# Kernel tuning notes

Measured on AMD Instinct MI355X. Metric: run time of the kernel, lower is better.

## Reference

```python
import jax, jax.numpy as jnp
import numpy as np

DIM = 768; HEADS = 12; N_PH = 4; EXPERTS = 8; TOPK = 2; EXPERT_DIM = 3072; MEM_HEADS = 8; EPS = 1e-5


def phm_linear(x, A, S, b):
    # PHM linear: W = sum_i kron(A[i] (n,n), S[i] (out/n, in/n)) -> (out, in); y = x @ W.T + b
    out_f = A.shape[1] * S.shape[1]
    in_f = A.shape[2] * S.shape[2]
    W = jnp.einsum('iab,icd->acbd', A, S).reshape(out_f, in_f)
    return x @ W.T + b


def layernorm(x, g, b):
    m = x.mean(-1, keepdims=True)
    v = x.var(-1, keepdims=True)
    return (x - m) / jnp.sqrt(v + EPS) * g + b


def quantum_attn(x, A_qkv, S_qkv, b_qkv, A_p, S_p, b_p, w_sup, w_ent):
    B, N, C = x.shape
    hd = C // HEADS
    qkv = phm_linear(x, A_qkv, S_qkv, b_qkv).reshape(B, N, 3, HEADS, hd)
    qkv = qkv.transpose(2, 0, 3, 1, 4)  # (3,B,H,N,hd)
    q, k, v = qkv[0], qkv[1], qkv[2]
    attn = jnp.einsum('bhnd,bhmd->bhnm', q, k) * (hd ** -0.5)
    # superposition head-mixing: sup[:,i] = sum_j w_sup[i,j] * attn[:,j]
    sup = jnp.einsum('ij,bjnm->binm', w_sup, attn)
    # entanglement: ent[:,i] = tanh(sup[:,i] + sum_j w_ent[i,j] * sup[:,j])
    ent = jnp.tanh(sup + jnp.einsum('ij,bjnm->binm', w_ent, sup))
    a = jax.nn.softmax(ent, axis=-1)
    o = jnp.einsum('bhnm,bhmd->bnhd', a, v).reshape(B, N, C)
    return phm_linear(o, A_p, S_p, b_p)


def moe(x, rA, rS, rb, domain_routing, domain_id, eA, eS, eb, ndw, ndb):
    logits = phm_linear(x, rA, rS, rb) + domain_routing[domain_id]  # (B,N,E)
    topv, topi = jax.lax.top_k(logits, TOPK)
    w = jax.nn.softmax(topv, axis=-1)  # (B,N,K)
    onehot = (topi[..., None] == jnp.arange(EXPERTS)).astype(x.dtype)  # (B,N,K,E)
    gates = jnp.einsum('bnk,bnke->bne', w, onehot)  # combined top-k gate per expert

    def expert(Ae, Se, be, We, bne):
        h = jax.nn.gelu(phm_linear(x, Ae, Se, be), approximate=False)
        return h @ We.T + bne

    outs = jax.vmap(expert)(eA, eS, eb, ndw, ndb)  # (E,B,N,C)
    return jnp.einsum('bne,ebnc->bnc', gates, outs)


def mem_mha(x, mem, iw, ib, ow, ob):
    # standard MHA: queries from x (B,N,C), keys/values from memory bank (M,C) shared across batch
    B, N, C = x.shape
    dh = C // MEM_HEADS
    q = (x @ iw[:C].T + ib[:C]).reshape(B, N, MEM_HEADS, dh)
    k = (mem @ iw[C:2 * C].T + ib[C:2 * C]).reshape(-1, MEM_HEADS, dh)
    v = (mem @ iw[2 * C:].T + ib[2 * C:]).reshape(-1, MEM_HEADS, dh)
    a = jax.nn.softmax(jnp.einsum('bnhd,mhd->bhnm', q, k) * (dh ** -0.5), axis=-1)
    o = jnp.einsum('bhnm,mhd->bnhd', a, v).reshape(B, N, C)
    return o @ ow.T + ob


def fractal(x, mems, iw, ib, ow, ob, pw, pb):
    # recursive FractalMemoryBank unrolled for depth=3:
    # level l: a_l = proc_l(MHA_l(prev, mem_l)); return prev + deeper(a_l)
    a0 = mem_mha(x, mems[0], iw[0], ib[0], ow[0], ob[0]) @ pw[0].T + pb[0]
    a1 = mem_mha(a0, mems[1], iw[1], ib[1], ow[1], ob[1]) @ pw[1].T + pb[1]
    a2 = mem_mha(a1, mems[2], iw[2], ib[2], ow[2], ob[2]) @ pw[2].T + pb[2]
    return x + (a0 + (a1 + a2))


def _fwd(x, ln1_g, ln1_b, attn_qkv_A, attn_qkv_S, attn_qkv_b, attn_proj_A, attn_proj_S, attn_proj_b,
         w_sup, w_ent, ln2_g, ln2_b, router_A, router_S, router_b, domain_routing,
         exp_A, exp_S, exp_b, exp_nd_w, exp_nd_b, mem0, mem1, mem2,
         mha_in_w, mha_in_b, mha_out_w, mha_out_b, proc_w, proc_b, ln3_g, ln3_b, domain_id):
    attended = x + quantum_attn(layernorm(x, ln1_g, ln1_b), attn_qkv_A, attn_qkv_S, attn_qkv_b,
                                attn_proj_A, attn_proj_S, attn_proj_b, w_sup, w_ent)
    moe_out = moe(layernorm(attended, ln2_g, ln2_b), router_A, router_S, router_b,
                  domain_routing, domain_id, exp_A, exp_S, exp_b, exp_nd_w, exp_nd_b)
    eo = attended + moe_out
    mo = fractal(eo, (mem0, mem1, mem2), mha_in_w, mha_in_b, mha_out_w, mha_out_b, proc_w, proc_b)
    return layernorm(mo, ln3_g, ln3_b)


def setup_inputs():
    key = jax.random.key(0)
    ks = iter(jax.random.split(key, 40))

    def rn(shape, s=0.02):
        return s * jax.random.normal(next(ks), shape, dtype=jnp.float32)

    B, N = 4, 512
    ones = jnp.ones(DIM, jnp.float32)
    zeros = jnp.zeros(DIM, jnp.float32)
    return {
        'x': rn((B, N, DIM), 1.0),
        'ln1_g': ones, 'ln1_b': zeros, 'ln2_g': ones, 'ln2_b': zeros, 'ln3_g': ones, 'ln3_b': zeros,
        'attn_qkv_A': rn((N_PH, N_PH, N_PH), 0.3),
        'attn_qkv_S': rn((N_PH, 3 * DIM // N_PH, DIM // N_PH)),
        'attn_qkv_b': jnp.zeros(3 * DIM, jnp.float32),
        'attn_proj_A': rn((N_PH, N_PH, N_PH), 0.3),
        'attn_proj_S': rn((N_PH, DIM // N_PH, DIM // N_PH)),
        'attn_proj_b': zeros,
        'w_sup': rn((HEADS, HEADS), 0.2), 'w_ent': rn((HEADS, HEADS), 0.2),
        'router_A': rn((N_PH, N_PH, N_PH), 0.3),
        'router_S': rn((N_PH, EXPERTS // N_PH, DIM // N_PH)),
        'router_b': jnp.zeros(EXPERTS, jnp.float32),
        'domain_routing': rn((6, EXPERTS), 1.0),
        'exp_A': rn((EXPERTS, N_PH, N_PH, N_PH), 0.3),
        'exp_S': rn((EXPERTS, N_PH, EXPERT_DIM // N_PH, DIM // N_PH)),
        'exp_b': jnp.zeros((EXPERTS, EXPERT_DIM), jnp.float32),
        'exp_nd_w': rn((EXPERTS, DIM, EXPERT_DIM)),
        'exp_nd_b': jnp.zeros((EXPERTS, DIM), jnp.float32),
        'mem0': rn((64, DIM), 1.0), 'mem1': rn((128, DIM), 1.0), 'mem2': rn((256, DIM), 1.0),
        'mha_in_w': rn((3, 3 * DIM, DIM)), 'mha_in_b': jnp.zeros((3, 3 * DIM), jnp.float32),
        'mha_out_w': rn((3, DIM, DIM)), 'mha_out_b': jnp.zeros((3, DIM), jnp.float32),
        'proc_w': rn((3, DIM, DIM)), 'proc_b': jnp.zeros((3, DIM), jnp.float32),
        'domain_id': 2,
    }


def reference(x, ln1_g, ln1_b, ln2_g, ln2_b, ln3_g, ln3_b, attn_qkv_A, attn_qkv_S, attn_qkv_b,
              attn_proj_A, attn_proj_S, attn_proj_b, w_sup, w_ent, router_A, router_S, router_b,
              domain_routing, exp_A, exp_S, exp_b, exp_nd_w, exp_nd_b, mem0, mem1, mem2,
              mha_in_w, mha_in_b, mha_out_w, mha_out_b, proc_w, proc_b, domain_id):
    return _fwd(x, ln1_g, ln1_b, attn_qkv_A, attn_qkv_S, attn_qkv_b, attn_proj_A, attn_proj_S,
                attn_proj_b, w_sup, w_ent, ln2_g, ln2_b, router_A, router_S, router_b,
                domain_routing, exp_A, exp_S, exp_b, exp_nd_w, exp_nd_b, mem0, mem1, mem2,
                mha_in_w, mha_in_b, mha_out_w, mha_out_b, proc_w, proc_b, ln3_g, ln3_b, domain_id)
```

## Files before the change

kernel.cpp:

```cpp
#include <hip/hip_runtime.h>
#include <math.h>

#define DIM    768
#define NTOK   2048
#define NSEQ   512
#define NBATCH 4
#define NHEADS 12
#define HD     64
#define QKVC   2304
#define MHEADS 8
#define MHD    96
#define NEXP   8
#define EDIM   3072
#define DD     (DIM*DIM)

typedef unsigned short u16;
typedef __attribute__((ext_vector_type(8))) short short8;
typedef __attribute__((ext_vector_type(4))) float f32x4;

struct L3 { long a, b, c; };
struct I3 { int a, b, c; };
struct CJ { const float4* s[6]; ushort4* d[6]; int n4[6]; };

__device__ __forceinline__ float gelu_exact(float v){
    return 0.5f * v * (1.f + erff(v * 0.70710678118654752f));
}
__device__ __forceinline__ u16 f2bf(float f){
    unsigned int u = __builtin_bit_cast(unsigned int, f);
    unsigned int r = (u + 0x7FFFu + ((u >> 16) & 1u)) >> 16;
    return (u16)r;
}
__device__ __forceinline__ float fast_tanh(float s){
    return 1.f - 2.f/(__expf(2.f*s) + 1.f);
}
__device__ __forceinline__ void gll16(const u16* g, u16* l){
    __builtin_amdgcn_global_load_lds((const __attribute__((address_space(1))) void*)g,
                                     (__attribute__((address_space(3))) void*)l, 16, 0, 0);
}

template<int WM,int WN,int FR>
__device__ __forceinline__ void mgemm_core(
    const u16* __restrict__ Xb, int ldx, int rowBase, int rowLim,
    const u16* __restrict__ Wb, int ldw, int colBase, int colLim, int K,
    const float* __restrict__ bias,
    const float* __restrict__ res, int ldres,
    float* __restrict__ Cf, u16* __restrict__ Cb, int ldc,
    float scale, int act)
{
    constexpr int TM = 16*FR;
    constexpr int RM = WM*TM, RN = WN*TM, NT = WM*WN*64;
    constexpr int IA = (RM*8)/NT, IB = (RN*8)/NT;
    __shared__ u16 As[2][RM*64];
    __shared__ u16 Bs[2][RN*64];
    int tid = threadIdx.x;
    int lane = tid & 63, w = tid >> 6;
    int wm = (w / WN) * TM, wn = (w % WN) * TM;
    const f32x4 zf = {0.f, 0.f, 0.f, 0.f};
    f32x4 acc[FR][FR];
    #pragma unroll
    for (int i=0;i<FR;i++)
        #pragma unroll
        for (int j=0;j<FR;j++) acc[i][j] = zf;

    const bool fullA = (rowBase + RM <= rowLim);
    const bool fullB = (colBase + RN <= colLim);
    const int nt = (K + 63) >> 6;

    auto stage = [&](int buf, int k0){
        const bool kfull = (k0 + 64 <= K);
        if (fullA && kfull) {
            #pragma unroll
            for (int it = 0; it < IA; ++it) {
                int idx = it*NT + tid;
                int r = idx >> 3, c = idx & 7;
                gll16(&Xb[(size_t)(rowBase + r)*ldx + k0 + ((c ^ (r & 7)) << 3)], &As[buf][(size_t)idx*8]);
            }
        } else {
            #pragma unroll
            for (int it = 0; it < IA; ++it) {
                int idx = it*NT + tid;
                int r = idx >> 3, c = idx & 7;
                int gr = rowBase + r;
                uint4 v = {0u,0u,0u,0u};
                if (gr < rowLim && (k0 + c*8) < K) v = *(const uint4*)&Xb[(size_t)gr*ldx + k0 + c*8];
                *(uint4*)&As[buf][r*64 + ((c ^ (r & 7)) * 8)] = v;
            }
        }
        if (fullB && kfull) {
            #pragma unroll
            for (int it = 0; it < IB; ++it) {
                int idx = it*NT + tid;
                int r = idx >> 3, c = idx & 7;
                gll16(&Wb[(size_t)(colBase + r)*ldw + k0 + ((c ^ (r & 7)) << 3)], &Bs[buf][(size_t)idx*8]);
            }
        } else {
            #pragma unroll
            for (int it = 0; it < IB; ++it) {
                int idx = it*NT + tid;
                int r = idx >> 3, c = idx & 7;
                int gc = colBase + r;
                uint4 v = {0u,0u,0u,0u};
                if (gc < colLim && (k0 + c*8) < K) v = *(const uint4*)&Wb[(size_t)gc*ldw + k0 + c*8];
                *(uint4*)&Bs[buf][r*64 + ((c ^ (r & 7)) * 8)] = v;
            }
        }
    };

    stage(0, 0);
    __syncthreads();
    for (int t = 0; t < nt; ++t) {
        if (t + 1 < nt) stage((t+1)&1, (t+1)*64);
        const u16* Ac = As[t&1];
        const u16* Bc = Bs[t&1];
        int lr = lane & 15, lk = lane >> 4;
        #pragma unroll
        for (int ks = 0; ks < 2; ++ks) {
            short8 af[FR], bfr[FR];
            #pragma unroll
            for (int mi=0; mi<FR; mi++){
                int row = wm + mi*16 + lr;
                int cidx = (ks*4 + lk) ^ (row & 7);
                af[mi] = *(const short8*)&Ac[row*64 + cidx*8];
            }
            #pragma unroll
            for (int ni=0; ni<FR; ni++){
                int col = wn + ni*16 + lr;
                int cidx = (ks*4 + lk) ^ (col & 7);
                bfr[ni] = *(const short8*)&Bc[col*64 + cidx*8];
            }
            #pragma unroll
            for (int mi=0; mi<FR; mi++)
                #pragma unroll
                for (int ni=0; ni<FR; ni++)
                    acc[mi][ni] = __builtin_amdgcn_mfma_f32_16x16x32_bf16(af[mi], bfr[ni], acc[mi][ni], 0, 0, 0);
        }
        __syncthreads();
    }
    int lr = lane & 15, lg = lane >> 4;
    #pragma unroll
    for (int mi=0; mi<FR; mi++){
        #pragma unroll
        for (int r=0; r<4; r++){
            int row = rowBase + wm + mi*16 + lg*4 + r;
            if (row >= rowLim) continue;
            #pragma unroll
            for (int ni=0; ni<FR; ni++){
                int col = colBase + wn + ni*16 + lr;
                if (col >= colLim) continue;
                float v = acc[mi][ni][r] * scale;
                if (bias) v += bias[col];
                if (act == 1) v = gelu_exact(v);
                if (Cb) Cb[(size_t)row*ldc + col] = f2bf(v);
                if (res) v += res[(size_t)row*ldres + col];
                if (Cf) Cf[(size_t)row*ldc + col] = v;
            }
        }
    }
}

template<int WM,int WN,int FR>
__global__ __launch_bounds__(WM*WN*64) void k_mgemm(
    const u16* __restrict__ X, int ldx, int M,
    const u16* __restrict__ W, int ldw, int N, int K,
    const float* __restrict__ bias, const float* __restrict__ res, int ldres,
    float* __restrict__ Cf, u16* __restrict__ Cb, int ldc, float scale, int act)
{
    constexpr int RM = WM*16*FR, RN = WN*16*FR;
    mgemm_core<WM,WN,FR>(X, ldx, blockIdx.x*RM, M, W, ldw, blockIdx.y*RN, N, K,
                         bias, res, ldres, Cf, Cb, ldc, scale, act);
}

template<int WM,int WN,int FR>
__global__ __launch_bounds__(WM*WN*64) void k_mgemm_b3(
    const u16* __restrict__ X, L3 xo, int ldx, I3 Mv,
    const u16* __restrict__ W, L3 wo, int ldw, int N, int K,
    const float* __restrict__ bias, L3 bo,
    u16* __restrict__ Cb, L3 co, int ldc, float scale, int act)
{
    constexpr int RM = WM*16*FR, RN = WN*16*FR;
    int z = blockIdx.z;
    int M    = (z==0) ? Mv.a : (z==1) ? Mv.b : Mv.c;
    long xof = (z==0) ? xo.a : (z==1) ? xo.b : xo.c;
    long wof = (z==0) ? wo.a : (z==1) ? wo.b : wo.c;
    long bof = (z==0) ? bo.a : (z==1) ? bo.b : bo.c;
    long cof = (z==0) ? co.a : (z==1) ? co.b : co.c;
    if ((int)blockIdx.x * RM >= M) return;
    mgemm_core<WM,WN,FR>(X + xof, ldx, blockIdx.x*RM, M, W + wof, ldw, blockIdx.y*RN, N, K,
                         bias ? bias + bof : nullptr, nullptr, 0, nullptr, Cb + cof, ldc, scale, act);
}

template<int WM,int WN,int FR>
__global__ __launch_bounds__(WM*WN*64) void k_mgemm_expert(
    const u16* __restrict__ X, int ldx,
    const u16* __restrict__ Wb, int ldw, long wStride,
    const float* __restrict__ biasB, int biasStride,
    const int* __restrict__ prefix, const int* __restrict__ cnt,
    float* __restrict__ Cf, u16* __restrict__ Cb, int ldc, int N, int K, int act)
{
    constexpr int RM = WM*16*FR, RN = WN*16*FR;
    int e = blockIdx.z;
    int n = cnt[e];
    if ((int)blockIdx.x * RM >= n) return;
    mgemm_core<WM,WN,FR>(X, ldx, prefix[e] + blockIdx.x*RM, prefix[e] + n,
                         Wb + (size_t)e*wStride, ldw, blockIdx.y*RN, N, K,
                         biasB + (size_t)e*biasStride, nullptr, 0, Cf, Cb, ldc, 1.f, act);
}

template<int WM,int WN,int FR>
__global__ __launch_bounds__(WM*WN*64) void k_mgemm_qk(const u16* __restrict__ qkv, float* __restrict__ attn)
{
    constexpr int RM = WM*16*FR, RN = WN*16*FR;
    int z = blockIdx.z, b = z / NHEADS, h = z % NHEADS;
    const u16* X = qkv + (size_t)b*NSEQ*QKVC + h*HD;
    const u16* W = qkv + (size_t)b*NSEQ*QKVC + DIM + h*HD;
    float* C = attn + (size_t)z*NSEQ*NSEQ;
    mgemm_core<WM,WN,FR>(X, QKVC, blockIdx.x*RM, NSEQ, W, QKVC, blockIdx.y*RN, NSEQ, HD,
                         nullptr, nullptr, 0, C, nullptr, NSEQ, 0.125f, 0);
}

template<int WM,int WN,int FR>
__global__ __launch_bounds__(WM*WN*64) void k_mgemm_pv(const u16* __restrict__ P, const u16* __restrict__ Vt, u16* __restrict__ o)
{
    constexpr int RM = WM*16*FR, RN = WN*16*FR;
    int z = blockIdx.z, b = z / NHEADS, h = z % NHEADS;
    const u16* X = P + (size_t)z*NSEQ*NSEQ;
    const u16* W = Vt + ((size_t)b*DIM + h*HD)*NSEQ;
    u16* C = o + (size_t)b*NSEQ*DIM + h*HD;
    mgemm_core<WM,WN,FR>(X, NSEQ, blockIdx.x*RM, NSEQ, W, NSEQ, blockIdx.y*RN, HD, NSEQ,
                         nullptr, nullptr, 0, nullptr, C, DIM, 1.f, 0);
}

template<int WM,int WN,int FR>
__global__ __launch_bounds__(WM*WN*64) void k_mgemm_memqk(const u16* __restrict__ q, const u16* __restrict__ k, int ldk,
                                                          float* __restrict__ S, int M, float scale)
{
    constexpr int RM = WM*16*FR, RN = WN*16*FR;
    int h = blockIdx.z;
    mgemm_core<WM,WN,FR>(q + h*MHD, DIM, blockIdx.x*RM, NTOK, k + h*MHD, ldk, blockIdx.y*RN, M, MHD,
                         nullptr, nullptr, 0, S + (size_t)h*NTOK*M, nullptr, M, scale, 0);
}

template<int WM,int WN,int FR>
__global__ __launch_bounds__(WM*WN*64) void k_mgemm_mempv(const u16* __restrict__ P, const u16* __restrict__ Vt,
                                                          u16* __restrict__ O, int M)
{
    constexpr int RM = WM*16*FR, RN = WN*16*FR;
    int h = blockIdx.z;
    mgemm_core<WM,WN,FR>(P + (size_t)h*NTOK*M, M, blockIdx.x*RM, NTOK, Vt + (size_t)h*MHD*M, M,
                         blockIdx.y*RN, MHD, M,
                         nullptr, nullptr, 0, nullptr, O + h*MHD, DIM, 1.f, 0);
}

__global__ __launch_bounds__(256) void k_transw_b(const u16* __restrict__ src, u16* __restrict__ dst)
{
    int z = blockIdx.y;
    int idx = blockIdx.x*256 + threadIdx.x;
    int r = idx / DIM, c = idx % DIM;
    dst[(size_t)z*DD + (size_t)c*DIM + r] = src[(size_t)z*DD + (size_t)r*DIM + c];
}

__global__ __launch_bounds__(256) void k_transvm_b(const u16* __restrict__ kvL, u16* __restrict__ Vtm3, I3 Mv)
{
    int z = blockIdx.y;
    int M = (z==0) ? Mv.a : (z==1) ? Mv.b : Mv.c;
    int idx = blockIdx.x*256 + threadIdx.x;
    if (idx >= DIM*M) return;
    int m = idx / DIM, d = idx % DIM;
    Vtm3[(size_t)z*DIM*256 + (size_t)d*M + m] = kvL[(size_t)z*256*2*DIM + (size_t)m*2*DIM + DIM + d];
}

__global__ __launch_bounds__(64) void k_softmax_mem(const float* __restrict__ S, u16* __restrict__ P, int M)
{
    size_t base = (size_t)blockIdx.x * M;
    int lane = threadIdx.x;
    float mx = -1e30f;
    for (int i = lane; i < M; i += 64) mx = fmaxf(mx, S[base+i]);
    for (int off=32; off; off>>=1) mx = fmaxf(mx, __shfl_xor(mx, off));
    float sum = 0.f;
    for (int i = lane; i < M; i += 64) sum += __expf(S[base+i]-mx);
    for (int off=32; off; off>>=1) sum += __shfl_xor(sum, off);
    float inv = 1.f/sum;
    for (int i = lane; i < M; i += 64) P[base+i] = f2bf(__expf(S[base+i]-mx)*inv);
}

__global__ __launch_bounds__(256) void k_phm(
    const float* __restrict__ A, const float* __restrict__ S, void* __restrict__ W,
    int So, int Si, int inF, long Astride, long Sstride, long Wstride, int obf)
{
    int e = blockIdx.y;
    const float* Ae = A + (size_t)e*Astride;
    const float* Se = S + (size_t)e*Sstride;
    size_t idx = (size_t)blockIdx.x*256 + threadIdx.x;
    size_t total = (size_t)(So*4) * inF;
    if (idx >= total) return;
    int in = (int)(idx % inF);
    int o  = (int)(idx / inF);
    int a = o / So, c = o % So, b = in / Si, d = in % Si;
    float w = 0.f;
    #pragma unroll
    for (int i=0;i<4;i++) w = fmaf(Ae[i*16 + a*4 + b], Se[((size_t)i*So + c)*Si + d], w);
    if (obf) ((u16*)W)[(size_t)e*Wstride + idx] = f2bf(w);
    else     ((float*)W)[(size_t)e*Wstride + idx] = w;
}

__global__ __launch_bounds__(256) void k_cvt4(const float4* __restrict__ s, ushort4* __restrict__ d, int n4)
{
    for (int i = blockIdx.x*256 + threadIdx.x; i < n4; i += gridDim.x*256){
        float4 v = s[i];
        ushort4 o; o.x = f2bf(v.x); o.y = f2bf(v.y); o.z = f2bf(v.z); o.w = f2bf(v.w);
        d[i] = o;
    }
}
__global__ __launch_bounds__(256) void k_cvt_multi(CJ J)
{
    int z = blockIdx.y;
    const float4* s = J.s[z]; ushort4* d = J.d[z]; int n4 = J.n4[z];
    for (int i = blockIdx.x*256 + threadIdx.x; i < n4; i += gridDim.x*256){
        float4 v = s[i];
        ushort4 o; o.x = f2bf(v.x); o.y = f2bf(v.y); o.z = f2bf(v.z); o.w = f2bf(v.w);
        d[i] = o;
    }
}

__global__ __launch_bounds__(256) void k_bc(const float* __restrict__ pw, const float* __restrict__ outb,
                                            const float* __restrict__ pb, float* __restrict__ bc)
{
    int l = blockIdx.y;
    int i = blockIdx.x*4 + (threadIdx.x >> 6);
    int lane = threadIdx.x & 63;
    const float* pr = pw + ((size_t)l*DIM + i)*DIM;
    const float* ob = outb + (size_t)l*DIM;
    float s = 0.f;
    for (int j = lane; j < DIM; j += 64) s = fmaf(pr[j], ob[j], s);
    for (int off=32; off; off>>=1) s += __shfl_xor(s, off);
    if (lane == 0) bc[(size_t)l*DIM + i] = s + pb[(size_t)l*DIM + i];
}

__global__ __launch_bounds__(256) void k_ln(const float* __restrict__ x, const float* __restrict__ g,
                                            const float* __restrict__ b,
                                            float* __restrict__ yf, u16* __restrict__ yb)
{
    int row = blockIdx.x, tid = threadIdx.x;
    const float* xr = x + (size_t)row * DIM;
    float v0 = xr[tid], v1 = xr[tid+256], v2 = xr[tid+512];
    float s = v0+v1+v2;
    float ss = v0*v0 + v1*v1 + v2*v2;
    for (int off=32; off; off>>=1){ s += __shfl_xor(s,off); ss += __shfl_xor(ss,off); }
    __shared__ float sa[4], sb[4];
    int wid = tid >> 6;
    if ((tid & 63) == 0){ sa[wid]=s; sb[wid]=ss; }
    __syncthreads();
    s  = sa[0]+sa[1]+sa[2]+sa[3];
    ss = sb[0]+sb[1]+sb[2]+sb[3];
    float mean = s * (1.f/DIM);
    float var  = ss * (1.f/DIM) - mean*mean;
    float rstd = rsqrtf(var + 1e-5f);
    float o0 = (v0-mean)*rstd*g[tid]     + b[tid];
    float o1 = (v1-mean)*rstd*g[tid+256] + b[tid+256];
    float o2 = (v2-mean)*rstd*g[tid+512] + b[tid+512];
    if (yf){ float* yr = yf + (size_t)row*DIM; yr[tid]=o0; yr[tid+256]=o1; yr[tid+512]=o2; }
    if (yb){ u16* yr = yb + (size_t)row*DIM; yr[tid]=f2bf(o0); yr[tid+256]=f2bf(o1); yr[tid+512]=f2bf(o2); }
}

__global__ __launch_bounds__(256) void k_supsoft(
    const float* __restrict__ attn, u16* __restrict__ P,
    const float* __restrict__ wsup, const float* __restrict__ went)
{
    __shared__ float S[NHEADS][NSEQ];
    __shared__ float ws[144], we[144];
    int bn = blockIdx.x;
    int b = bn >> 9, n = bn & 511;
    int tid = threadIdx.x;
    if (tid < 144){ ws[tid] = wsup[tid]; we[tid] = went[tid]; }
    size_t base = ((size_t)b*NHEADS*NSEQ + n)*NSEQ;
    #pragma unroll
    for (int it=0; it<24; ++it){
        int idx = it*256 + tid;
        int j = idx >> 9, m = idx & 511;
        S[j][m] = attn[base + (size_t)j*NSEQ*NSEQ + m];
    }
    __syncthreads();
    #pragma unroll
    for (int half=0; half<2; ++half){
        int m = tid + half*256;
        float av[12], sup[12];
        #pragma unroll
        for (int j=0;j<12;j++) av[j] = S[j][m];
        #pragma unroll
        for (int i=0;i<12;i++){
            float s = 0.f;
            #pragma unroll
            for (int j=0;j<12;j++) s = fmaf(ws[i*12+j], av[j], s);
            sup[i] = s;
        }
        #pragma unroll
        for (int i=0;i<12;i++){
            float s = sup[i];
            #pragma unroll
            for (int j=0;j<12;j++) s = fmaf(we[i*12+j], sup[j], s);
            av[i] = fast_tanh(s);
        }
        #pragma unroll
        for (int i=0;i<12;i++) S[i][m] = av[i];
    }
    __syncthreads();
    int lane = tid & 63, wv = tid >> 6;
    #pragma unroll
    for (int jj=0; jj<3; ++jj){
        int j = wv*3 + jj;
        float v[8], mx = -1e30f;
        #pragma unroll
        for (int k=0;k<8;k++){ v[k] = S[j][lane + 64*k]; mx = fmaxf(mx, v[k]); }
        for (int off=32; off; off>>=1) mx = fmaxf(mx, __shfl_xor(mx, off));
        float sum = 0.f;
        #pragma unroll
        for (int k=0;k<8;k++){ v[k] = __expf(v[k]-mx); sum += v[k]; }
        for (int off=32; off; off>>=1) sum += __shfl_xor(sum, off);
        float inv = 1.f/sum;
        #pragma unroll
        for (int k=0;k<8;k++) P[base + (size_t)j*NSEQ*NSEQ + lane + 64*k] = f2bf(v[k]*inv);
    }
}

__global__ __launch_bounds__(256) void k_transv(const u16* __restrict__ qkv, u16* __restrict__ Vt)
{
    __shared__ u16 L[64][65];
    int mt = blockIdx.x*64, dt = blockIdx.y*64, b = blockIdx.z;
    int tid = threadIdx.x;
    #pragma unroll
    for (int it=0; it<16; ++it){
        int idx = it*256 + tid;
        int mm = idx >> 6, dd = idx & 63;
        L[mm][dd] = qkv[((size_t)b*NSEQ + mt + mm)*QKVC + 1536 + dt + dd];
    }
    __syncthreads();
    #pragma unroll
    for (int it=0; it<16; ++it){
        int idx = it*256 + tid;
        int dd = idx >> 6, mm = idx & 63;
        Vt[((size_t)b*DIM + dt + dd)*NSEQ + mt + mm] = L[mm][dd];
    }
}

__global__ __launch_bounds__(256) void k_route(
    const float* __restrict__ ln2, const float* __restrict__ Wr,
    const float* __restrict__ rb, const float* __restrict__ dr,
    const int* __restrict__ did, int* __restrict__ topi, float* __restrict__ topw, int* __restrict__ cnt)
{
    int t = blockIdx.x, tid = threadIdx.x;
    const float* xr = ln2 + (size_t)t*DIM;
    float a[8] = {};
    #pragma unroll
    for (int ii=0; ii<3; ii++){
        int i = tid + ii*256;
        float xv = xr[i];
        #pragma unroll
        for (int e=0;e<8;e++) a[e] = fmaf(xv, Wr[e*DIM + i], a[e]);
    }
    #pragma unroll
    for (int e=0;e<8;e++)
        for (int off=32; off; off>>=1) a[e] += __shfl_xor(a[e], off);
    __shared__ float sred[4][8];
// ... 44 lines not shown
    }
}

__global__ __launch_bounds__(256) void k_gather(const u16* __restrict__ src, const int* __restrict__ tokof, u16* __restrict__ dst)
{
    int i = blockIdx.x*256 + threadIdx.x;
    int row = i / 96, c = (i % 96) * 8;
    *(uint4*)&dst[(size_t)row*DIM + c] = *(const uint4*)&src[(size_t)tokof[row]*DIM + c];
}

__global__ __launch_bounds__(256) void k_combine(
    const float* __restrict__ att, const float* __restrict__ outg,
    const int* __restrict__ rowof, const float* __restrict__ topw,
    float* __restrict__ eo, u16* __restrict__ eob)
{
    size_t i = (size_t)blockIdx.x*256 + threadIdx.x;
    int t = (int)(i / DIM), c = (int)(i % DIM);
    int r0 = rowof[2*t], r1 = rowof[2*t+1];
    float v = att[i] + topw[2*t]*outg[(size_t)r0*DIM+c] + topw[2*t+1]*outg[(size_t)r1*DIM+c];
    eo[i] = v;
    eob[i] = f2bf(v);
}

extern "C" void kernel_launch(void* const* d_in, const int* in_sizes, int n_in,
                              void* d_out, int out_size, void* d_ws, size_t ws_size,
                              hipStream_t stream)
{
    const float* x     = (const float*)d_in[0];
    const float* ln1g  = (const float*)d_in[1];
    const float* ln1b  = (const float*)d_in[2];
    const float* ln2g  = (const float*)d_in[3];
    const float* ln2b  = (const float*)d_in[4];
    const float* ln3g  = (const float*)d_in[5];
    const float* ln3b  = (const float*)d_in[6];
    const float* qkvA  = (const float*)d_in[7];
    const float* qkvS  = (const float*)d_in[8];
    const float* qkvb  = (const float*)d_in[9];
    const float* projA = (const float*)d_in[10];
    const float* projS = (const float*)d_in[11];
    const float* projb = (const float*)d_in[12];
    const float* wsup  = (const float*)d_in[13];
    const float* went  = (const float*)d_in[14];
    const float* rA    = (const float*)d_in[15];
    const float* rS    = (const float*)d_in[16];
    const float* rb    = (const float*)d_in[17];
    const float* dr    = (const float*)d_in[18];
    const float* eA    = (const float*)d_in[19];
    const float* eS    = (const float*)d_in[20];
    const float* eb    = (const float*)d_in[21];
    const float* ndw   = (const float*)d_in[22];
    const float* ndb   = (const float*)d_in[23];
    const float* mem0  = (const float*)d_in[24];
    const float* mem1  = (const float*)d_in[25];
    const float* mem2  = (const float*)d_in[26];
    const float* inw   = (const float*)d_in[27];
    const float* inb   = (const float*)d_in[28];
    const float* outw  = (const float*)d_in[29];
    const float* outb  = (const float*)d_in[30];
    const float* pw    = (const float*)d_in[31];
    const float* pb    = (const float*)d_in[32];
    const int*   did   = (const int*)d_in[33];

    float* f = (float*)d_ws;
    size_t off = 0;
    auto alloc = [&](size_t n){ float* p = f + off; off += (n + 3) & ~(size_t)3; return p; };
    auto allocb = [&](size_t n){ return (u16*)alloc((n + 1) / 2); };

    float* lnbuf  = alloc((size_t)NTOK*DIM);
    float* attnd  = alloc((size_t)NTOK*DIM);
    float* eo     = alloc((size_t)NTOK*DIM);
    float* accum  = alloc((size_t)NTOK*DIM);
    float* attnb  = alloc((size_t)48*NSEQ*NSEQ);
    float* Wrout  = alloc((size_t)NEXP*DIM);
    float* topw   = alloc((size_t)2*NTOK);
    float* bcb    = alloc((size_t)3*DIM);
    int* ip = (int*)alloc((size_t)6*NTOK + 64);
    int* topi   = ip;            ip += 2*NTOK;
    int* rowof  = ip;            ip += 2*NTOK;
    int* tokof  = ip;            ip += 2*NTOK;
    int* cnt    = ip;            ip += 8;
    int* cnt2   = ip;            ip += 8;
    int* prefix = ip;            ip += 8;

    float* outg   = attnb;
    u16*   ndw_bf = (u16*)(attnb + (size_t)3146240);
    float* Smem   = attnb;

    u16* Wqkv_bf  = allocb((size_t)QKVC*DIM);
    u16* Wproj_bf = allocb((size_t)DD);
    u16* Wexp_bf  = allocb((size_t)NEXP*EDIM*DIM);
    u16* inw_bf   = allocb((size_t)3*QKVC*DIM);
    u16* outw_bf  = allocb((size_t)3*DD);
    u16* pw_bf    = allocb((size_t)3*DD);
    u16* Wc_bf    = allocb((size_t)3*DD);
    u16* wT3_bf   = allocb((size_t)3*DD);
    u16* mem_bf   = allocb((size_t)448*DIM);
    u16* qkv_bf   = allocb((size_t)NTOK*QKVC);
    u16* Vt_bf    = allocb((size_t)NBATCH*DIM*NSEQ);
    u16* P_bf     = allocb((size_t)48*NSEQ*NSEQ);
    u16* lnx_bf   = allocb((size_t)NTOK*DIM);
    u16* o_bf     = allocb((size_t)NTOK*DIM);
    u16* inx_bf   = allocb((size_t)NTOK*DIM);
    u16* mhao_bf  = allocb((size_t)NTOK*DIM);
    u16* kvL_bf   = allocb((size_t)3*256*2*DIM);
    u16* Vtm3_bf  = allocb((size_t)3*DIM*256);
    u16* Xg_bf    = qkv_bf;
    u16* hidden_bf= P_bf;
    u16* Pm_bf    = P_bf;
    u16* qm_bf    = o_bf;

    float* outf = (float*)d_out;
    dim3 T256(256), T64(64);
    I3 Ms3 = {64, 128, 256};

    k_zero<<<1, 32, 0, stream>>>(cnt, 16);
    k_ln<<<NTOK, T256, 0, stream>>>(x, ln1g, ln1b, nullptr, lnx_bf);
    k_phm<<<dim3((QKVC*DIM+255)/256,1), T256, 0, stream>>>(qkvA, qkvS, Wqkv_bf, 576, 192, DIM, 0,0,0, 1);
    k_phm<<<dim3((DD+255)/256,1),  T256, 0, stream>>>(projA, projS, Wproj_bf, 192, 192, DIM, 0,0,0, 1);
    k_phm<<<dim3((NEXP*DIM+255)/256,1), T256, 0, stream>>>(rA, rS, Wrout, 2, 192, DIM, 0,0,0, 0);
    k_phm<<<dim3((EDIM*DIM+255)/256,NEXP), T256, 0, stream>>>(eA, eS, Wexp_bf, 768, 192, DIM,
                                                              64L, (long)4*768*192, (long)EDIM*DIM, 1);
    {
        CJ J;
        J.s[0]=(const float4*)inw;  J.d[0]=(ushort4*)inw_bf;  J.n4[0]=3*QKVC*DIM/4;
        J.s[1]=(const float4*)outw; J.d[1]=(ushort4*)outw_bf; J.n4[1]=3*DD/4;
        J.s[2]=(const float4*)pw;   J.d[2]=(ushort4*)pw_bf;   J.n4[2]=3*DD/4;
        J.s[3]=(const float4*)mem0; J.d[3]=(ushort4*)mem_bf;              J.n4[3]=64*DIM/4;
        J.s[4]=(const float4*)mem1; J.d[4]=(ushort4*)(mem_bf + 64*DIM);   J.n4[4]=128*DIM/4;
        J.s[5]=(const float4*)mem2; J.d[5]=(ushort4*)(mem_bf + 192*DIM);  J.n4[5]=256*DIM/4;
        k_cvt_multi<<<dim3(1024, 6), T256, 0, stream>>>(J);
    }
    k_bc<<<dim3(DIM/4, 3), T256, 0, stream>>>(pw, outb, pb, bcb);
    k_transw_b<<<dim3(DD/256, 3), T256, 0, stream>>>(outw_bf, wT3_bf);
    {
        L3 dd3 = {0, DD, 2*DD}, z3 = {0,0,0};
        I3 m768 = {DIM, DIM, DIM};
        k_mgemm_b3<2,2,2><<<dim3(12,12,3), T256, 0, stream>>>(pw_bf, dd3, DIM, m768,
                                                              wT3_bf, dd3, DIM, DIM, DIM,
                                                              nullptr, z3, Wc_bf, dd3, DIM, 1.f, 0);
    }
    {
        L3 xo = {0, 64L*DIM, 192L*DIM};
        L3 wo = {(long)DD, (long)QKVC*DIM + DD, 2L*QKVC*DIM + DD};
        L3 bo = {(long)DIM, (long)QKVC + DIM, 2L*QKVC + DIM};
        L3 co = {0, 256L*2*DIM, 2*256L*2*DIM};
        k_mgemm_b3<1,1,2><<<dim3(8,48,3), T64, 0, stream>>>(mem_bf, xo, DIM, Ms3,
                                                            inw_bf, wo, DIM, 2*DIM, DIM,
                                                            inb, bo, kvL_bf, co, 2*DIM, 1.f, 0);
    }
    k_transvm_b<<<dim3((DIM*256)/256, 3), T256, 0, stream>>>(kvL_bf, Vtm3_bf, Ms3);

    k_mgemm<2,2,4><<<dim3(16,18), T256, 0, stream>>>(lnx_bf, DIM, NTOK, Wqkv_bf, DIM, QKVC, DIM,
                                                     qkvb, nullptr, 0, nullptr, qkv_bf, QKVC, 1.f, 0);
    k_transv<<<dim3(8,12,NBATCH), T256, 0, stream>>>(qkv_bf, Vt_bf);
    k_mgemm_qk<2,2,4><<<dim3(4,4,48), T256, 0, stream>>>(qkv_bf, attnb);
    k_supsoft<<<dim3(NTOK), T256, 0, stream>>>(attnb, P_bf, wsup, went);
    k_cvt4<<<4096, T256, 0, stream>>>((const float4*)ndw, (ushort4*)ndw_bf, NEXP*DIM*EDIM/4);
    k_mgemm_pv<1,1,2><<<dim3(16,2,48), T64, 0, stream>>>(P_bf, Vt_bf, o_bf);
    k_mgemm<2,2,2><<<dim3(32,12), T256, 0, stream>>>(o_bf, DIM, NTOK, Wproj_bf, DIM, DIM, DIM,
                                                     projb, x, DIM, attnd, nullptr, DIM, 1.f, 0);
    k_ln<<<NTOK, T256, 0, stream>>>(attnd, ln2g, ln2b, lnbuf, lnx_bf);
    k_route<<<NTOK, T256, 0, stream>>>(lnbuf, Wrout, rb, dr, did, topi, topw, cnt);
    k_prefix<<<1, 1, 0, stream>>>(cnt, prefix);
    k_assign<<<8, T256, 0, stream>>>(topi, prefix, cnt2, rowof, tokof);
    k_gather<<<dim3(1536), T256, 0, stream>>>(lnx_bf, tokof, Xg_bf);
    k_mgemm_expert<2,2,4><<<dim3(16,24,NEXP), T256, 0, stream>>>(Xg_bf, DIM, Wexp_bf, DIM, (long)EDIM*DIM,
                                                                 eb, EDIM, prefix, cnt,
                                                                 nullptr, hidden_bf, EDIM, EDIM, DIM, 1);
    k_mgemm_expert<2,2,2><<<dim3(32,12,NEXP), T256, 0, stream>>>(hidden_bf, EDIM, ndw_bf, EDIM, (long)DIM*EDIM,
                                                                 ndb, DIM, prefix, cnt,
                                                                 outg, nullptr, DIM, DIM, EDIM, 0);
    k_combine<<<dim3(6144), T256, 0, stream>>>(attnd, outg, rowof, topw, eo, inx_bf);
    int Ms[3] = {64, 128, 256};
    for (int l=0; l<3; ++l){
        const u16* iwl = inw_bf + (size_t)l*QKVC*DIM;
        int M = Ms[l];
        k_mgemm<2,2,2><<<dim3(32,12), T256, 0, stream>>>(inx_bf, DIM, NTOK, iwl, DIM, DIM, DIM,
                                                         inb + (size_t)l*QKVC, nullptr, 0, nullptr, qm_bf, DIM, 1.f, 0);
        k_mgemm_memqk<1,1,2><<<dim3(64, M/32, MHEADS), T64, 0, stream>>>(qm_bf, kvL_bf + (size_t)l*256*2*DIM, 2*DIM,
                                                                         Smem, M, 0.10206207261596577f);
        k_softmax_mem<<<dim3(MHEADS*NTOK), T64, 0, stream>>>(Smem, Pm_bf, M);
        k_mgemm_mempv<1,1,2><<<dim3(64,3,MHEADS), T64, 0, stream>>>(Pm_bf, Vtm3_bf + (size_t)l*DIM*256, mhao_bf, M);
        k_mgemm<2,2,2><<<dim3(32,12), T256, 0, stream>>>(mhao_bf, DIM, NTOK, Wc_bf + (size_t)l*DD, DIM, DIM, DIM,
                                                         bcb + (size_t)l*DIM, (l==0 ? eo : accum), DIM,
                                                         accum, inx_bf, DIM, 1.f, 0);
    }
    k_ln<<<NTOK, T256, 0, stream>>>(accum, ln3g, ln3b, outf, nullptr);
}
```

Before: 716.8 us.

## Fuse memory-attention QK with softmax, store attention scores as bf16, add single-buffer GEMM option

A new kernel fuses the memory-bank QK^T GEMM with the row softmax. It does the reduction across waves through shared memory and writes bf16 probabilities directly, so the fp32 score buffer and the separate softmax launch go away. The QK attention scores are now written as bf16 instead of fp32, which halves the traffic into k_supsoft but adds rounding before the head-mixing and tanh. The GEMM core also gets a template flag for single-buffered LDS, used for the large 2x2x4 tiles to cut shared memory and allow higher occupancy, at the cost of losing load/compute overlap.

```diff
diff --git a/kernel.cpp b/kernel.cpp
--- a/kernel.cpp
+++ b/kernel.cpp
@@ -30,6 +30,10 @@
     unsigned int r = (u + 0x7FFFu + ((u >> 16) & 1u)) >> 16;
     return (u16)r;
 }
+__device__ __forceinline__ float bf2f(u16 b){
+    unsigned int u = ((unsigned int)b) << 16;
+    return __builtin_bit_cast(float, u);
+}
 __device__ __forceinline__ float fast_tanh(float s){
     return 1.f - 2.f/(__expf(2.f*s) + 1.f);
 }
@@ -38,7 +42,7 @@
                                      (__attribute__((address_space(3))) void*)l, 16, 0, 0);
 }
 
-template<int WM,int WN,int FR>
+template<int WM,int WN,int FR,int DB>
 __device__ __forceinline__ void mgemm_core(
     const u16* __restrict__ Xb, int ldx, int rowBase, int rowLim,
     const u16* __restrict__ Wb, int ldw, int colBase, int colLim, int K,
@@ -50,8 +54,9 @@
     constexpr int TM = 16*FR;
     constexpr int RM = WM*TM, RN = WN*TM, NT = WM*WN*64;
     constexpr int IA = (RM*8)/NT, IB = (RN*8)/NT;
-    __shared__ u16 As[2][RM*64];
-    __shared__ u16 Bs[2][RN*64];
+    constexpr int NB = DB ? 2 : 1;
+    __shared__ u16 As[NB][RM*64];
+    __shared__ u16 Bs[NB][RN*64];
     int tid = threadIdx.x;
     int lane = tid & 63, w = tid >> 6;
     int wm = (w / WN) * TM, wn = (w % WN) * TM;
@@ -65,6 +70,7 @@
     const bool fullA = (rowBase + RM <= rowLim);
     const bool fullB = (colBase + RN <= colLim);
     const int nt = (K + 63) >> 6;
+    int lr = lane & 15, lk = lane >> 4;
 
     auto stage = [&](int buf, int k0){
         const bool kfull = (k0 + 64 <= K);
@@ -105,14 +111,7 @@
             }
         }
     };
-
-    stage(0, 0);
-    __syncthreads();
-    for (int t = 0; t < nt; ++t) {
-        if (t + 1 < nt) stage((t+1)&1, (t+1)*64);
-        const u16* Ac = As[t&1];
-        const u16* Bc = Bs[t&1];
-        int lr = lane & 15, lk = lane >> 4;
+    auto compute = [&](const u16* Ac, const u16* Bc){
         #pragma unroll
         for (int ks = 0; ks < 2; ++ks) {
             short8 af[FR], bfr[FR];
@@ -134,9 +133,25 @@
                 for (int ni=0; ni<FR; ni++)
                     acc[mi][ni] = __builtin_amdgcn_mfma_f32_16x16x32_bf16(af[mi], bfr[ni], acc[mi][ni], 0, 0, 0);
         }
+    };
+
+    if (DB) {
+        stage(0, 0);
         __syncthreads();
-    }
-    int lr = lane & 15, lg = lane >> 4;
+        for (int t = 0; t < nt; ++t) {
+            if (t + 1 < nt) stage((t+1)&1, (t+1)*64);
+            compute(As[t&1], Bs[t&1]);
+            __syncthreads();
+        }
+    } else {
+        for (int t = 0; t < nt; ++t) {
+            stage(0, t*64);
+            __syncthreads();
+            compute(As[0], Bs[0]);
+            __syncthreads();
+        }
+    }
+    int lg = lane >> 4;
     #pragma unroll
     for (int mi=0; mi<FR; mi++){
         #pragma unroll
@@ -158,7 +173,7 @@
     }
 }
 
-template<int WM,int WN,int FR>
+template<int WM,int WN,int FR,int DB>
 __global__ __launch_bounds__(WM*WN*64) void k_mgemm(
     const u16* __restrict__ X, int ldx, int M,
     const u16* __restrict__ W, int ldw, int N, int K,
@@ -166,11 +181,11 @@
     float* __restrict__ Cf, u16* __restrict__ Cb, int ldc, float scale, int act)
 {
     constexpr int RM = WM*16*FR, RN = WN*16*FR;
-    mgemm_core<WM,WN,FR>(X, ldx, blockIdx.x*RM, M, W, ldw, blockIdx.y*RN, N, K,
-                         bias, res, ldres, Cf, Cb, ldc, scale, act);
-}
-
-template<int WM,int WN,int FR>
+    mgemm_core<WM,WN,FR,DB>(X, ldx, blockIdx.x*RM, M, W, ldw, blockIdx.y*RN, N, K,
+                            bias, res, ldres, Cf, Cb, ldc, scale, act);
+}
+
+template<int WM,int WN,int FR,int DB>
 __global__ __launch_bounds__(WM*WN*64) void k_mgemm_b3(
     const u16* __restrict__ X, L3 xo, int ldx, I3 Mv,
     const u16* __restrict__ W, L3 wo, int ldw, int N, int K,
@@ -185,11 +200,11 @@
     long bof = (z==0) ? bo.a : (z==1) ? bo.b : bo.c;
     long cof = (z==0) ? co.a : (z==1) ? co.b : co.c;
     if ((int)blockIdx.x * RM >= M) return;
-    mgemm_core<WM,WN,FR>(X + xof, ldx, blockIdx.x*RM, M, W + wof, ldw, blockIdx.y*RN, N, K,
-                         bias ? bias + bof : nullptr, nullptr, 0, nullptr, Cb + cof, ldc, scale, act);
-}
-
-template<int WM,int WN,int FR>
+    mgemm_core<WM,WN,FR,DB>(X + xof, ldx, blockIdx.x*RM, M, W + wof, ldw, blockIdx.y*RN, N, K,
+                            bias ? bias + bof : nullptr, nullptr, 0, nullptr, Cb + cof, ldc, scale, act);
+}
+
+template<int WM,int WN,int FR,int DB>
 __global__ __launch_bounds__(WM*WN*64) void k_mgemm_expert(
     const u16* __restrict__ X, int ldx,
     const u16* __restrict__ Wb, int ldw, long wStride,
@@ -201,24 +216,24 @@
     int e = blockIdx.z;
     int n = cnt[e];
     if ((int)blockIdx.x * RM >= n) return;
-    mgemm_core<WM,WN,FR>(X, ldx, prefix[e] + blockIdx.x*RM, prefix[e] + n,
-                         Wb + (size_t)e*wStride, ldw, blockIdx.y*RN, N, K,
-                         biasB + (size_t)e*biasStride, nullptr, 0, Cf, Cb, ldc, 1.f, act);
-}
-
-template<int WM,int WN,int FR>
-__global__ __launch_bounds__(WM*WN*64) void k_mgemm_qk(const u16* __restrict__ qkv, float* __restrict__ attn)
+    mgemm_core<WM,WN,FR,DB>(X, ldx, prefix[e] + blockIdx.x*RM, prefix[e] + n,
+                            Wb + (size_t)e*wStride, ldw, blockIdx.y*RN, N, K,
+                            biasB + (size_t)e*biasStride, nullptr, 0, Cf, Cb, ldc, 1.f, act);
+}
+
+template<int WM,int WN,int FR,int DB>
+__global__ __launch_bounds__(WM*WN*64) void k_mgemm_qk(const u16* __restrict__ qkv, u16* __restrict__ attn)
 {
     constexpr int RM = WM*16*FR, RN = WN*16*FR;
     int z = blockIdx.z, b = z / NHEADS, h = z % NHEADS;
     const u16* X = qkv + (size_t)b*NSEQ*QKVC + h*HD;
     const u16* W = qkv + (size_t)b*NSEQ*QKVC + DIM + h*HD;
-    float* C = attn + (size_t)z*NSEQ*NSEQ;
-    mgemm_core<WM,WN,FR>(X, QKVC, blockIdx.x*RM, NSEQ, W, QKVC, blockIdx.y*RN, NSEQ, HD,
-                         nullptr, nullptr, 0, C, nullptr, NSEQ, 0.125f, 0);
-}
-
-template<int WM,int WN,int FR>
+    u16* C = attn + (size_t)z*NSEQ*NSEQ;
+    mgemm_core<WM,WN,FR,DB>(X, QKVC, blockIdx.x*RM, NSEQ, W, QKVC, blockIdx.y*RN, NSEQ, HD,
+                            nullptr, nullptr, 0, nullptr, C, NSEQ, 0.125f, 0);
+}
+
+template<int WM,int WN,int FR,int DB>
 __global__ __launch_bounds__(WM*WN*64) void k_mgemm_pv(const u16* __restrict__ P, const u16* __restrict__ Vt, u16* __restrict__ o)
 {
     constexpr int RM = WM*16*FR, RN = WN*16*FR;
@@ -226,29 +241,167 @@
     const u16* X = P + (size_t)z*NSEQ*NSEQ;
     const u16* W = Vt + ((size_t)b*DIM + h*HD)*NSEQ;
     u16* C = o + (size_t)b*NSEQ*DIM + h*HD;
-    mgemm_core<WM,WN,FR>(X, NSEQ, blockIdx.x*RM, NSEQ, W, NSEQ, blockIdx.y*RN, HD, NSEQ,
-                         nullptr, nullptr, 0, nullptr, C, DIM, 1.f, 0);
-}
-
-template<int WM,int WN,int FR>
-__global__ __launch_bounds__(WM*WN*64) void k_mgemm_memqk(const u16* __restrict__ q, const u16* __restrict__ k, int ldk,
-                                                          float* __restrict__ S, int M, float scale)
+    mgemm_core<WM,WN,FR,DB>(X, NSEQ, blockIdx.x*RM, NSEQ, W, NSEQ, blockIdx.y*RN, HD, NSEQ,
+                            nullptr, nullptr, 0, nullptr, C, DIM, 1.f, 0);
+}
+
+template<int WM,int WN,int FR,int DB>
+__global__ __launch_bounds__(WM*WN*64) void k_mgemm_mempv(const u16* __restrict__ P, const u16* __restrict__ Vt,
+                                                          u16* __restrict__ O, int M)
 {
     constexpr int RM = WM*16*FR, RN = WN*16*FR;
     int h = blockIdx.z;
-    mgemm_core<WM,WN,FR>(q + h*MHD, DIM, blockIdx.x*RM, NTOK, k + h*MHD, ldk, blockIdx.y*RN, M, MHD,
-                         nullptr, nullptr, 0, S + (size_t)h*NTOK*M, nullptr, M, scale, 0);
-}
-
-template<int WM,int WN,int FR>
-__global__ __launch_bounds__(WM*WN*64) void k_mgemm_mempv(const u16* __restrict__ P, const u16* __restrict__ Vt,
-                                                          u16* __restrict__ O, int M)
-{
-    constexpr int RM = WM*16*FR, RN = WN*16*FR;
-    int h = blockIdx.z;
-    mgemm_core<WM,WN,FR>(P + (size_t)h*NTOK*M, M, blockIdx.x*RM, NTOK, Vt + (size_t)h*MHD*M, M,
-                         blockIdx.y*RN, MHD, M,
-                         nullptr, nullptr, 0, nullptr, O + h*MHD, DIM, 1.f, 0);
+    mgemm_core<WM,WN,FR,DB>(P + (size_t)h*NTOK*M, M, blockIdx.x*RM, NTOK, Vt + (size_t)h*MHD*M, M,
+                            blockIdx.y*RN, MHD, M,
+                            nullptr, nullptr, 0, nullptr, O + h*MHD, DIM, 1.f, 0);
+}
+
+__global__ __launch_bounds__(256) void k_memqk_soft(
+    const u16* __restrict__ q, const u16* __restrict__ kv, int ldk,
+    u16* __restrict__ P, int M, float scale)
+{
+    constexpr int RM = 64, RN = 256, NT = 256, K = MHD;
+    __shared__ u16 As[RM*64];
+    __shared__ u16 Bs[RN*64];
+    __shared__ float red0[RM][4];
+    __shared__ float red1[RM][4];
+    int h = blockIdx.y;
+    int rowBase = blockIdx.x * RM;
+    const u16* Xb = q + h*MHD;
+    const u16* Wb = kv + h*MHD;
+    int tid = threadIdx.x, lane = tid & 63, w = tid >> 6;
+    int wn = w * 64;
+    int lr = lane & 15, lk = lane >> 4;
+    const f32x4 zf = {0.f,0.f,0.f,0.f};
+    f32x4 acc[4][4];
+    #pragma unroll
+    for (int i=0;i<4;i++)
+        #pragma unroll
+        for (int j=0;j<4;j++) acc[i][j] = zf;
+
+    for (int k0 = 0; k0 < K; k0 += 64) {
+        const bool kfull = (k0 + 64 <= K);
+        if (kfull) {
+            #pragma unroll
+            for (int it = 0; it < 2; ++it) {
+                int idx = it*NT + tid;
+                int r = idx >> 3, c = idx & 7;
+                gll16(&Xb[(size_t)(rowBase + r)*DIM + k0 + ((c ^ (r & 7)) << 3)], &As[(size_t)idx*8]);
+            }
+        } else {
+            #pragma unroll
+            for (int it = 0; it < 2; ++it) {
+                int idx = it*NT + tid;
+                int r = idx >> 3, c = idx & 7;
+                uint4 v = {0u,0u,0u,0u};
+                if ((k0 + c*8) < K) v = *(const uint4*)&Xb[(size_t)(rowBase + r)*DIM + k0 + c*8];
+                *(uint4*)&As[r*64 + ((c ^ (r & 7)) * 8)] = v;
+            }
+        }
+        #pragma unroll
+        for (int it = 0; it < 8; ++it) {
+            int idx = it*NT + tid;
+            int r = idx >> 3, c = idx & 7;
+            uint4 v = {0u,0u,0u,0u};
+            if (r < M && (k0 + c*8) < K) v = *(const uint4*)&Wb[(size_t)r*ldk + k0 + c*8];
+            *(uint4*)&Bs[r*64 + ((c ^ (r & 7)) * 8)] = v;
+        }
+        __syncthreads();
+        #pragma unroll
+        for (int ks = 0; ks < 2; ++ks) {
+            short8 af[4], bfr[4];
+            #pragma unroll
+            for (int mi=0; mi<4; mi++){
+                int row = mi*16 + lr;
+                int cidx = (ks*4 + lk) ^ (row & 7);
+                af[mi] = *(const short8*)&As[row*64 + cidx*8];
+            }
+            #pragma unroll
+            for (int ni=0; ni<4; ni++){
+                int col = wn + ni*16 + lr;
+                int cidx = (ks*4 + lk) ^ (col & 7);
+                bfr[ni] = *(const short8*)&Bs[col*64 + cidx*8];
+            }
+            #pragma unroll
+            for (int mi=0; mi<4; mi++)
+                #pragma unroll
+                for (int ni=0; ni<4; ni++)
+                    acc[mi][ni] = __builtin_amdgcn_mfma_f32_16x16x32_bf16(af[mi], bfr[ni], acc[mi][ni], 0, 0, 0);
+        }
+        __syncthreads();
+    }
+    int lg = lane >> 4;
+    float sc[4][4][4];
+    float rmax[4][4];
+    #pragma unroll
+    for (int mi=0; mi<4; mi++){
+        #pragma unroll
+        for (int r=0; r<4; r++){
+            float m = -1e30f;
+            #pragma unroll
+            for (int ni=0; ni<4; ni++){
+                int col = wn + ni*16 + lr;
+                float v = (col < M) ? acc[mi][ni][r]*scale : -1e30f;
+                sc[mi][r][ni] = v;
+                m = fmaxf(m, v);
+            }
+            m = fmaxf(m, __shfl_xor(m, 1));
+            m = fmaxf(m, __shfl_xor(m, 2));
+            m = fmaxf(m, __shfl_xor(m, 4));
+            m = fmaxf(m, __shfl_xor(m, 8));
+            rmax[mi][r] = m;
+        }
+    }
+    if (lr == 0){
+        #pragma unroll
+        for (int mi=0; mi<4; mi++)
+            #pragma unroll
+            for (int r=0; r<4; r++) red0[mi*16 + lg*4 + r][w] = rmax[mi][r];
+    }
+    __syncthreads();
+    float gmax[4][4], rsum[4][4];
+    #pragma unroll
+    for (int mi=0; mi<4; mi++){
+        #pragma unroll
+        for (int r=0; r<4; r++){
+            int row = mi*16 + lg*4 + r;
+            float g = fmaxf(fmaxf(red0[row][0], red0[row][1]), fmaxf(red0[row][2], red0[row][3]));
+            gmax[mi][r] = g;
+            float s = 0.f;
+            #pragma unroll
+            for (int ni=0; ni<4; ni++){
+                int col = wn + ni*16 + lr;
+                if (col < M) s += __expf(sc[mi][r][ni] - g);
+            }
+            s += __shfl_xor(s, 1);
+            s += __shfl_xor(s, 2);
+            s += __shfl_xor(s, 4);
+            s += __shfl_xor(s, 8);
+            rsum[mi][r] = s;
+        }
+    }
+    if (lr == 0){
+        #pragma unroll
+        for (int mi=0; mi<4; mi++)
+            #pragma unroll
+            for (int r=0; r<4; r++) red1[mi*16 + lg*4 + r][w] = rsum[mi][r];
+    }
+    __syncthreads();
+    #pragma unroll
+    for (int mi=0; mi<4; mi++){
+        #pragma unroll
+        for (int r=0; r<4; r++){
+            int row = mi*16 + lg*4 + r;
+            float tot = red1[row][0] + red1[row][1] + red1[row][2] + red1[row][3];
+            float inv = 1.f / tot;
+            #pragma unroll
+            for (int ni=0; ni<4; ni++){
+                int col = wn + ni*16 + lr;
+                if (col < M)
+                    P[((size_t)h*NTOK + rowBase + row)*M + col] = f2bf(__expf(sc[mi][r][ni] - gmax[mi][r]) * inv);
+            }
+        }
+    }
 }
 
 __global__ __launch_bounds__(256) void k_transw_b(const u16* __restrict__ src, u16* __restrict__ dst)
@@ -267,20 +420,6 @@
     if (idx >= DIM*M) return;
     int m = idx / DIM, d = idx % DIM;
     Vtm3[(size_t)z*DIM*256 + (size_t)d*M + m] = kvL[(size_t)z*256*2*DIM + (size_t)m*2*DIM + DIM + d];
-}
-
-__global__ __launch_bounds__(64) void k_softmax_mem(const float* __restrict__ S, u16* __restrict__ P, int M)
-{
-    size_t base = (size_t)blockIdx.x * M;
-    int lane = threadIdx.x;
-    float mx = -1e30f;
-    for (int i = lane; i < M; i += 64) mx = fmaxf(mx, S[base+i]);
-    for (int off=32; off; off>>=1) mx = fmaxf(mx, __shfl_xor(mx, off));
-    float sum = 0.f;
-    for (int i = lane; i < M; i += 64) sum += __expf(S[base+i]-mx);
-    for (int off=32; off; off>>=1) sum += __shfl_xor(sum, off);
-    float inv = 1.f/sum;
-    for (int i = lane; i < M; i += 64) P[base+i] = f2bf(__expf(S[base+i]-mx)*inv);
 }
 
 __global__ __launch_bounds__(256) void k_phm(
@@ -363,7 +502,7 @@
 }
 
 __global__ __launch_bounds__(256) void k_supsoft(
-    const float* __restrict__ attn, u16* __restrict__ P,
+    const u16* __restrict__ attn, u16* __restrict__ P,
     const float* __restrict__ wsup, const float* __restrict__ went)
 {
     __shared__ float S[NHEADS][NSEQ];
@@ -374,10 +513,12 @@
     if (tid < 144){ ws[tid] = wsup[tid]; we[tid] = went[tid]; }
     size_t base = ((size_t)b*NHEADS*NSEQ + n)*NSEQ;
     #pragma unroll
-    for (int it=0; it<24; ++it){
+    for (int it=0; it<12; ++it){
         int idx = it*256 + tid;
-        int j = idx >> 9, m = idx & 511;
-        S[j][m] = attn[base + (size_t)j*NSEQ*NSEQ + m];
+        int j = idx >> 8, m2 = (idx & 255) * 2;
+        unsigned int v = *(const unsigned int*)&attn[base + (size_t)j*NSEQ*NSEQ + m2];
+        S[j][m2]   = bf2f((u16)(v & 0xFFFFu));
+        S[j][m2+1] = bf2f((u16)(v >> 16));
     }
     __syncthreads();
     #pragma unroll
@@ -588,9 +729,9 @@
     int* cnt2   = ip;            ip += 8;
     int* prefix = ip;            ip += 8;
 
+    u16*   scores = (u16*)attnb;
     float* outg   = attnb;
     u16*   ndw_bf = (u16*)(attnb + (size_t)3146240);
-    float* Smem   = attnb;
 
     u16* Wqkv_bf  = allocb((size_t)QKVC*DIM);
     u16* Wproj_bf = allocb((size_t)DD);
@@ -641,55 +782,54 @@
     {
         L3 dd3 = {0, DD, 2*DD}, z3 = {0,0,0};
         I3 m768 = {DIM, DIM, DIM};
-        k_mgemm_b3<2,2,2><<<dim3(12,12,3), T256, 0, stream>>>(pw_bf, dd3, DIM, m768,
-                                                              wT3_bf, dd3, DIM, DIM, DIM,
-                                                              nullptr, z3, Wc_bf, dd3, DIM, 1.f, 0);
+        k_mgemm_b3<2,2,2,1><<<dim3(12,12,3), T256, 0, stream>>>(pw_bf, dd3, DIM, m768,
+                                                                wT3_bf, dd3, DIM, DIM, DIM,
+                                                                nullptr, z3, Wc_bf, dd3, DIM, 1.f, 0);
     }
     {
         L3 xo = {0, 64L*DIM, 192L*DIM};
         L3 wo = {(long)DD, (long)QKVC*DIM + DD, 2L*QKVC*DIM + DD};
         L3 bo = {(long)DIM, (long)QKVC + DIM, 2L*QKVC + DIM};
         L3 co = {0, 256L*2*DIM, 2*256L*2*DIM};
-        k_mgemm_b3<1,1,2><<<dim3(8,48,3), T64, 0, stream>>>(mem_bf, xo, DIM, Ms3,
-                                                            inw_bf, wo, DIM, 2*DIM, DIM,
-                                                            inb, bo, kvL_bf, co, 2*DIM, 1.f, 0);
+        k_mgemm_b3<1,1,2,1><<<dim3(8,48,3), T64, 0, stream>>>(mem_bf, xo, DIM, Ms3,
+                                                              inw_bf, wo, DIM, 2*DIM, DIM,
+                                                              inb, bo, kvL_bf, co, 2*DIM, 1.f, 0);
     }
     k_transvm_b<<<dim3((DIM*256)/256, 3), T256, 0, stream>>>(kvL_bf, Vtm3_bf, Ms3);
 
-    k_mgemm<2,2,4><<<dim3(16,18), T256, 0, stream>>>(lnx_bf, DIM, NTOK, Wqkv_bf, DIM, QKVC, DIM,
-                                                     qkvb, nullptr, 0, nullptr, qkv_bf, QKVC, 1.f, 0);
+    k_mgemm<2,2,4,0><<<dim3(16,18), T256, 0, stream>>>(lnx_bf, DIM, NTOK, Wqkv_bf, DIM, QKVC, DIM,
+                                                       qkvb, nullptr, 0, nullptr, qkv_bf, QKVC, 1.f, 0);
     k_transv<<<dim3(8,12,NBATCH), T256, 0, stream>>>(qkv_bf, Vt_bf);
-    k_mgemm_qk<2,2,4><<<dim3(4,4,48), T256, 0, stream>>>(qkv_bf, attnb);
-    k_supsoft<<<dim3(NTOK), T256, 0, stream>>>(attnb, P_bf, wsup, went);
+    k_mgemm_qk<2,2,4,0><<<dim3(4,4,48), T256, 0, stream>>>(qkv_bf, scores);
+    k_supsoft<<<dim3(NTOK), T256, 0, stream>>>(scores, P_bf, wsup, went);
     k_cvt4<<<4096, T256, 0, stream>>>((const float4*)ndw, (ushort4*)ndw_bf, NEXP*DIM*EDIM/4);
-    k_mgemm_pv<1,1,2><<<dim3(16,2,48), T64, 0, stream>>>(P_bf, Vt_bf, o_bf);
-    k_mgemm<2,2,2><<<dim3(32,12), T256, 0, stream>>>(o_bf, DIM, NTOK, Wproj_bf, DIM, DIM, DIM,
-                                                     projb, x, DIM, attnd, nullptr, DIM, 1.f, 0);
+    k_mgemm_pv<1,1,2,1><<<dim3(16,2,48), T64, 0, stream>>>(P_bf, Vt_bf, o_bf);
+    k_mgemm<2,2,2,1><<<dim3(32,12), T256, 0, stream>>>(o_bf, DIM, NTOK, Wproj_bf, DIM, DIM, DIM,
+                                                       projb, x, DIM, attnd, nullptr, DIM, 1.f, 0);
     k_ln<<<NTOK, T256, 0, stream>>>(attnd, ln2g, ln2b, lnbuf, lnx_bf);
     k_route<<<NTOK, T256, 0, stream>>>(lnbuf, Wrout, rb, dr, did, topi, topw, cnt);
     k_prefix<<<1, 1, 0, stream>>>(cnt, prefix);
     k_assign<<<8, T256, 0, stream>>>(topi, prefix, cnt2, rowof, tokof);
     k_gather<<<dim3(1536), T256, 0, stream>>>(lnx_bf, tokof, Xg_bf);
-    k_mgemm_expert<2,2,4><<<dim3(16,24,NEXP), T256, 0, stream>>>(Xg_bf, DIM, Wexp_bf, DIM, (long)EDIM*DIM,
-                                                                 eb, EDIM, prefix, cnt,
-                                                                 nullptr, hidden_bf, EDIM, EDIM, DIM, 1);
-    k_mgemm_expert<2,2,2><<<dim3(32,12,NEXP), T256, 0, stream>>>(hidden_bf, EDIM, ndw_bf, EDIM, (long)DIM*EDIM,
-                                                                 ndb, DIM, prefix, cnt,
-                                                                 outg, nullptr, DIM, DIM, EDIM, 0);
+    k_mgemm_expert<2,2,4,0><<<dim3(16,24,NEXP), T256, 0, stream>>>(Xg_bf, DIM, Wexp_bf, DIM, (long)EDIM*DIM,
+                                                                   eb, EDIM, prefix, cnt,
+                                                                   nullptr, hidden_bf, EDIM, EDIM, DIM, 1);
+    k_mgemm_expert<2,2,2,1><<<dim3(32,12,NEXP), T256, 0, stream>>>(hidden_bf, EDIM, ndw_bf, EDIM, (long)DIM*EDIM,
+                                                                   ndb, DIM, prefix, cnt,
+                                                                   outg, nullptr, DIM, DIM, EDIM, 0);
     k_combine<<<dim3(6144), T256, 0, stream>>>(attnd, outg, rowof, topw, eo, inx_bf);
     int Ms[3] = {64, 128, 256};
     for (int l=0; l<3; ++l){
         const u16* iwl = inw_bf + (size_t)l*QKVC*DIM;
         int M = Ms[l];
-        k_mgemm<2,2,2><<<dim3(32,12), T256, 0, stream>>>(inx_bf, DIM, NTOK, iwl, DIM, DIM, DIM,
-                                                         inb + (size_t)l*QKVC, nullptr, 0, nullptr, qm_bf, DIM, 1.f, 0);
-        k_mgemm_memqk<1,1,2><<<dim3(64, M/32, MHEADS), T64, 0, stream>>>(qm_bf, kvL_bf + (size_t)l*256*2*DIM, 2*DIM,
-                                                                         Smem, M, 0.10206207261596577f);
-        k_softmax_mem<<<dim3(MHEADS*NTOK), T64, 0, stream>>>(Smem, Pm_bf, M);
-        k_mgemm_mempv<1,1,2><<<dim3(64,3,MHEADS), T64, 0, stream>>>(Pm_bf, Vtm3_bf + (size_t)l*DIM*256, mhao_bf, M);
-        k_mgemm<2,2,2><<<dim3(32,12), T256, 0, stream>>>(mhao_bf, DIM, NTOK, Wc_bf + (size_t)l*DD, DIM, DIM, DIM,
-                                                         bcb + (size_t)l*DIM, (l==0 ? eo : accum), DIM,
-                                                         accum, inx_bf, DIM, 1.f, 0);
+        k_mgemm<2,2,2,1><<<dim3(32,12), T256, 0, stream>>>(inx_bf, DIM, NTOK, iwl, DIM, DIM, DIM,
+                                                           inb + (size_t)l*QKVC, nullptr, 0, nullptr, qm_bf, DIM, 1.f, 0);
+        k_memqk_soft<<<dim3(NTOK/64, MHEADS), T256, 0, stream>>>(qm_bf, kvL_bf + (size_t)l*256*2*DIM, 2*DIM,
+                                                                 Pm_bf, M, 0.10206207261596577f);
+        k_mgemm_mempv<1,1,2,1><<<dim3(64,3,MHEADS), T64, 0, stream>>>(Pm_bf, Vtm3_bf + (size_t)l*DIM*256, mhao_bf, M);
+        k_mgemm<2,2,2,1><<<dim3(32,12), T256, 0, stream>>>(mhao_bf, DIM, NTOK, Wc_bf + (size_t)l*DD, DIM, DIM, DIM,
+                                                           bcb + (size_t)l*DIM, (l==0 ? eo : accum), DIM,
+                                                           accum, inx_bf, DIM, 1.f, 0);
     }
     k_ln<<<NTOK, T256, 0, stream>>>(accum, ln3g, ln3b, outf, nullptr);
 }
```

Measured after the change: 686.0 us. -4.3%, faster.
